# Kernel optimization log

Measured on AMD Instinct MI355X. Metric: run time of the kernel, lower is better.

## Reference

```python
import jax, jax.numpy as jnp
import numpy as np

D_MODEL, N_HEAD, D_HEAD, D_INNER = 1024, 16, 64, 4096
QLEN, MLEN, BATCH = 1024, 1024, 2
KLEN = QLEN + MLEN
LN_EPS = 1e-5


def layer_norm(x, g, b):
    m = jnp.mean(x, axis=-1, keepdims=True)
    v = jnp.mean((x - m) ** 2, axis=-1, keepdims=True)
    return g * (x - m) * jax.lax.rsqrt(v + LN_EPS) + b


def rel_shift(x):
    # x: [q, k, b, n] -> Transformer-XL relative shift
    q, k = x.shape[0], x.shape[1]
    zero_pad = jnp.zeros((q, 1) + x.shape[2:], dtype=x.dtype)
    x_padded = jnp.concatenate([zero_pad, x], axis=1)          # [q, k+1, b, n]
    x_padded = x_padded.reshape((k + 1, q) + x.shape[2:])      # [k+1, q, b, n]
    return x_padded[1:].reshape(x.shape)


def setup_inputs() -> dict:
    key = jax.random.key(0)
    ks = jax.random.split(key, 12)
    s = 0.02
    return {
        "w": jax.random.normal(ks[0], (QLEN, BATCH, D_MODEL), jnp.float32),
        "mems": jax.random.normal(ks[1], (MLEN, BATCH, D_MODEL), jnp.float32),
        "r_emb": jax.random.normal(ks[2], (KLEN, N_HEAD, D_HEAD), jnp.float32) * s,
        "r_w_bias": jax.random.normal(ks[3], (N_HEAD, D_HEAD), jnp.float32) * s,
        "r_bias": jax.random.normal(ks[4], (KLEN, N_HEAD), jnp.float32) * s,
        "qkv_w": jax.random.normal(ks[5], (3 * N_HEAD * D_HEAD, D_MODEL), jnp.float32) * s,
        "o_w": jax.random.normal(ks[6], (D_MODEL, N_HEAD * D_HEAD), jnp.float32) * s,
        "ln1_g": jnp.ones((D_MODEL,), jnp.float32),
        "ln1_b": jnp.zeros((D_MODEL,), jnp.float32),
        "ff_w1": jax.random.normal(ks[7], (D_INNER, D_MODEL), jnp.float32) * s,
        "ff_b1": jnp.zeros((D_INNER,), jnp.float32),
        "ff_w2": jax.random.normal(ks[8], (D_MODEL, D_INNER), jnp.float32) * s,
        "ff_b2": jnp.zeros((D_MODEL,), jnp.float32),
        "ln2_g": jnp.ones((D_MODEL,), jnp.float32),
        "ln2_b": jnp.zeros((D_MODEL,), jnp.float32),
    }


def reference(w, mems, r_emb, r_w_bias, r_bias, qkv_w, o_w, ln1_g, ln1_b,
              ff_w1, ff_b1, ff_w2, ff_b2, ln2_g, ln2_b):
    qlen, nbatch = w.shape[0], w.shape[1]
    scale = 1.0 / (D_HEAD ** 0.5)

    # --- RelLearnableMultiHeadAttn (post-lnorm, dropout=0 / eval) ---
    cat = jnp.concatenate([mems, w], axis=0)                       # [klen, b, d_model]
    w_heads = jnp.einsum('kbd,ed->kbe', cat, qkv_w)                # [klen, b, 3*n*h]
    w_head_q, w_head_k, w_head_v = jnp.split(w_heads, 3, axis=-1)
    klen = w_head_k.shape[0]
    w_head_q = w_head_q[-qlen:].reshape(qlen, nbatch, N_HEAD, D_HEAD)
    w_head_k = w_head_k.reshape(klen, nbatch, N_HEAD, D_HEAD)
    w_head_v = w_head_v.reshape(klen, nbatch, N_HEAD, D_HEAD)

    r_emb_k = r_emb[-klen:]                                        # [klen, n, h]
    r_bias_k = r_bias[-klen:]                                      # [klen, n]

    rw_head_q = w_head_q + r_w_bias[None, None]                    # [q, b, n, h]
    AC = jnp.einsum('ibnd,jbnd->ijbn', rw_head_q, w_head_k)        # [q, k, b, n]
    B_ = jnp.einsum('ibnd,jnd->ijbn', w_head_q, r_emb_k)           # [q, k, b, n]
    D_ = r_bias_k[None, :, None, :]                                # [1, k, 1, n]
    BD = rel_shift(B_ + D_)

    attn_score = (AC + BD) * scale
    # causal mask with memory: key j attendable iff j <= i + mlen
    mlen = klen - qlen
    i = jnp.arange(qlen)[:, None]
    j = jnp.arange(klen)[None, :]
    mask = j > (i + mlen)                                          # [q, k]
    attn_score = jnp.where(mask[:, :, None, None], -1e30, attn_score)

    attn_prob = jax.nn.softmax(attn_score, axis=1)
    attn_vec = jnp.einsum('ijbn,jbnd->ibnd', attn_prob, w_head_v)
    attn_vec = attn_vec.reshape(qlen, nbatch, N_HEAD * D_HEAD)
    attn_out = jnp.einsum('ibe,de->ibd', attn_vec, o_w)
    h = layer_norm(w + attn_out, ln1_g, ln1_b)

    # --- PositionwiseFF (post-lnorm) ---
    inner = jax.nn.relu(jnp.einsum('ibd,fd->ibf', h, ff_w1) + ff_b1)
    ff_out = jnp.einsum('ibf,df->ibd', inner, ff_w2) + ff_b2
    out = layer_norm(h + ff_out, ln2_g, ln2_b)
    return out
```

## Files before the change

### kernel.cpp

```cpp
#include <hip/hip_runtime.h>
#include <math.h>

#define DM    1024
#define NH    16
#define DH    64
#define DI    4096
#define QL    1024
#define MLN   1024
#define BATCH 2
#define KL    2048
#define RPAD  2304

typedef unsigned short u16;
typedef short s16x8 __attribute__((ext_vector_type(8)));
typedef float f32x4 __attribute__((ext_vector_type(4)));

__device__ __forceinline__ u16 f2bf(float f) {
    union { float f; unsigned u; } v; v.f = f;
    unsigned u = v.u;
    unsigned r = (u + 0x7FFFu + ((u >> 16) & 1u)) >> 16;
    return (u16)r;
}
__device__ __forceinline__ u16 f2bf_fast(float f) {
    union { float f; unsigned u; } v; v.f = f;
    return (u16)((v.u + 0x8000u) >> 16);
}
__device__ __forceinline__ float bf2f(u16 h) {
    union { unsigned u; float f; } v; v.u = ((unsigned)h) << 16;
    return v.f;
}

__device__ __forceinline__ void gl2lds16(const void* g, void* l) {
    __builtin_amdgcn_global_load_lds(
        (const __attribute__((address_space(1))) void*)g,
        (__attribute__((address_space(3))) void*)l, 16, 0, 0);
}

__global__ __launch_bounds__(256) void cvt_multi(
    const float* __restrict__ a0, const float* __restrict__ a1,
    const float* __restrict__ a2, const float* __restrict__ a3,
    u16* __restrict__ o0, u16* __restrict__ o1,
    u16* __restrict__ o2, u16* __restrict__ o3) {
    int i = blockIdx.x * 256 + threadIdx.x;
    int stride = gridDim.x * 256;
    for (; i < 3145728; i += stride) {
        const float* src; u16* dst; int k;
        if (i < 786432)       { src = a0; dst = o0; k = i; }
        else if (i < 1048576) { src = a1; dst = o1; k = i - 786432; }
        else if (i < 2097152) { src = a2; dst = o2; k = i - 1048576; }
        else                  { src = a3; dst = o3; k = i - 2097152; }
        float4 v = ((const float4*)src)[k];
        ushort4 o = {f2bf(v.x), f2bf(v.y), f2bf(v.z), f2bf(v.w)};
        ((ushort4*)dst)[k] = o;
    }
}

__global__ __launch_bounds__(256) void cvt_cat(const float* __restrict__ mems,
                                               const float* __restrict__ w,
                                               u16* __restrict__ cat) {
    int id = blockIdx.x * 256 + threadIdx.x;
    int c4 = (id & 255) * 4;
    int row = id >> 8;
    int b = row >> 11, kpos = row & 2047;
    const float* src = (kpos < QL)
        ? mems + ((size_t)kpos * BATCH + b) * DM + c4
        : w + ((size_t)(kpos - QL) * BATCH + b) * DM + c4;
    float4 v = *(const float4*)src;
    ushort4 o = {f2bf(v.x), f2bf(v.y), f2bf(v.z), f2bf(v.w)};
    *(ushort4*)(cat + (size_t)row * DM + c4) = o;
}

__global__ __launch_bounds__(256) void rcvt(const float* __restrict__ r_emb,
                                            u16* __restrict__ rh) {
    int id = blockIdx.x * 256 + threadIdx.x;
    int n = blockIdx.y;
    int jj = id >> 3, gs = id & 7;
    s16x8 o;
    if (jj < KL) {
        int gl = (gs - jj) & 7;
        const float* s = r_emb + (size_t)jj * DM + n * 64 + gl * 8;
#pragma unroll
        for (int k = 0; k < 8; ++k) o[k] = (short)f2bf(s[k]);
    } else {
#pragma unroll
        for (int k = 0; k < 8; ++k) o[k] = 0;
    }
    *(s16x8*)(rh + ((size_t)n * RPAD + jj) * 64 + gs * 8) = o;
}

__global__ __launch_bounds__(256) void rb2_prep(const float* __restrict__ r_emb,
                                                const float* __restrict__ r_w_bias,
                                                const float* __restrict__ r_bias,
                                                float* __restrict__ rb2) {
    int jj = blockIdx.x * 256 + threadIdx.x;
    int n = blockIdx.y;
    if (jj >= RPAD) return;
    float v = 0.0f;
    if (jj < KL) {
        float dot = 0.0f;
#pragma unroll 8
        for (int d = 0; d < 64; ++d)
            dot += r_w_bias[n * 64 + d] * r_emb[(size_t)jj * DM + n * 64 + d];
        v = 0.125f * (r_bias[jj * NH + n] - dot);
    }
    rb2[n * RPAD + jj] = v;
}

template <int BN, int FLAGS>
__global__ __launch_bounds__(256) void gemm_s(const u16* __restrict__ A,
                                              const u16* __restrict__ B,
                                              float* __restrict__ Cf,
                                              u16* __restrict__ Cb,
                                              u16* __restrict__ Qo,
                                              u16* __restrict__ Ko,
                                              u16* __restrict__ Vo,
                                              const float* __restrict__ bias,
                                              int M, int N_out, int K) {
    constexpr int WN = BN / 2;
    constexpr int TN = WN / 16;
    __shared__ u16 As[128 * 32];
    __shared__ u16 Bs[BN * 32];

    const int t = threadIdx.x;
    const int lane = t & 63, wid = t >> 6;
    const int wm = wid >> 1, wn = wid & 1;
    const int lr = lane & 15, quad = lane >> 4;
    const int m_blk = blockIdx.y * 128;
    const int n_blk = blockIdx.x * BN;
    const int srow = t >> 2;
    const int skc  = (t & 3) * 8;

    f32x4 acc[4][TN];
#pragma unroll
    for (int i = 0; i < 4; ++i)
#pragma unroll
        for (int j = 0; j < TN; ++j) acc[i][j] = (f32x4)0.0f;

    for (int k0 = 0; k0 < K; k0 += 32) {
        __syncthreads();
        gl2lds16(A + (size_t)(m_blk + srow) * K + k0 + skc, As + wid * 512);
        gl2lds16(A + (size_t)(m_blk + 64 + srow) * K + k0 + skc, As + 2048 + wid * 512);
        gl2lds16(B + (size_t)(n_blk + srow) * K + k0 + skc, Bs + wid * 512);
        if (BN == 128)
            gl2lds16(B + (size_t)(n_blk + 64 + srow) * K + k0 + skc, Bs + 2048 + wid * 512);
        __syncthreads();

        s16x8 a[4], b[TN];
#pragma unroll
        for (int i = 0; i < 4; ++i)
            a[i] = *(const s16x8*)(As + (wm * 64 + i * 16 + lr) * 32 + quad * 8);
#pragma unroll
        for (int j = 0; j < TN; ++j)
            b[j] = *(const s16x8*)(Bs + (wn * WN + j * 16 + lr) * 32 + quad * 8);
#pragma unroll
        for (int i = 0; i < 4; ++i)
#pragma unroll
            for (int j = 0; j < TN; ++j)
                acc[i][j] = __builtin_amdgcn_mfma_f32_16x16x32_bf16(
                    a[i], b[j], acc[i][j], 0, 0, 0);
    }

#pragma unroll
    for (int i = 0; i < 4; ++i) {
#pragma unroll
        for (int j = 0; j < TN; ++j) {
            int row0 = m_blk + wm * 64 + i * 16 + quad * 4;
            int col  = n_blk + wn * WN + j * 16 + lr;
            if (FLAGS & 8) {
                int b_ = row0 >> 11, kpos = row0 & 2047;
                if (col < 1024) {
                    if (kpos >= QL) {
                        u16* q = Qo + ((size_t)(b_ * QL + kpos - QL)) * 1024 + col;
#pragma unroll
                        for (int r = 0; r < 4; ++r) q[r * 1024] = f2bf(acc[i][j][r]);
                    }
                } else if (col < 2048) {
                    int d = col & 63, nh = (col >> 6) & 15;
                    size_t base = ((size_t)((b_ * 16 + nh) * 16 + (kpos >> 7))) * 8192;
#pragma unroll
                    for (int r = 0; r < 4; ++r) {
                        int jl = (kpos & 127) + r;
                        Ko[base + jl * 64 + (((d >> 3) + jl) & 7) * 8 + (d & 7)] =
                            f2bf(acc[i][j][r]);
                    }
                } else {
                    int d = col & 63, nh = (col >> 6) & 15;
                    int jl = kpos & 127;
                    size_t base = ((size_t)((b_ * 16 + nh) * 16 + (kpos >> 7))) * 8192
                                  + d * 128 + (((jl >> 3) + d) & 15) * 8 + (jl & 7);
                    ushort4 o = {f2bf(acc[i][j][0]), f2bf(acc[i][j][1]),
                                 f2bf(acc[i][j][2]), f2bf(acc[i][j][3])};
                    *(ushort4*)(Vo + base) = o;
                }
            } else {
                float bv = (FLAGS & 2) ? bias[col] : 0.0f;
#pragma unroll
                for (int r = 0; r < 4; ++r) {
                    float v = acc[i][j][r] + bv;
                    if (FLAGS & 4) v = fmaxf(v, 0.0f);
                    size_t idx = (size_t)(row0 + r) * N_out + col;
                    if (FLAGS & 1) Cb[idx] = f2bf(v);
                    else           Cf[idx] = v;
                }
            }
        }
    }
}

__global__ __launch_bounds__(256, 2) void flash_attn(
    const u16* __restrict__ Qb, const u16* __restrict__ Kh,
    const u16* __restrict__ Vt2, const u16* __restrict__ rh,
    const float* __restrict__ r_w_bias, const float* __restrict__ rb2,
    u16* __restrict__ av) {
    const int bn = blockIdx.x & 31;
    const int i0 = (blockIdx.x >> 5) * 64;
    const int b = bn >> 4, n = bn & 15;
    const int t = threadIdx.x;
    const int lane = t & 63, w = t >> 6;
    const int lr = lane & 15, quad = lane >> 4;

    __shared__ __align__(16) u16 Ks[128 * 64];
    __shared__ __align__(16) u16 Vs[64 * 128];
    __shared__ __align__(16) u16 Rs[192 * 64];
    __shared__ __align__(16) u16 Pw_all[4 * 16 * 136];
    u16* Pw = Pw_all + w * (16 * 136);

    const int wrow0 = i0 + w * 16;

    s16x8 qw[2];
#pragma unroll
    for (int ks = 0; ks < 2; ++ks) {
        const u16* qp = Qb + ((size_t)(b * QL + wrow0 + lr)) * 1024 + n * 64 + ks * 32 + quad * 8;
        s16x8 qv = *(const s16x8*)qp;
        s16x8 o;
#pragma unroll
        for (int k = 0; k < 8; ++k) {
            float f = bf2f((u16)qv[k]) + r_w_bias[n * 64 + ks * 32 + quad * 8 + k];
            o[k] = (short)f2bf(f * 0.125f);
        }
        qw[ks] = o;
    }

    f32x4 O[4];
    float m_r[4], l_r[4];
#pragma unroll
    for (int x = 0; x < 4; ++x) {
        O[x] = (f32x4)0.0f;
        m_r[x] = -INFINITY;
        l_r[x] = 0.0f;
    }

    const u16* Kt0 = Kh + (size_t)bn * 16 * 8192;
    const u16* Vt0 = Vt2 + (size_t)bn * 16 * 8192;
    const int jend = i0 + 64 + MLN;

    for (int j0 = 0; j0 < jend; j0 += 128) {
        const int jjbase_blk = j0 + 960 - i0;
        __syncthreads();
        {
            const u16* Ksrc = Kt0 + (size_t)(j0 >> 7) * 8192;
            const u16* Vsrc = Vt0 + (size_t)(j0 >> 7) * 8192;
            const u16* Rsrc = rh + ((size_t)n * RPAD + jjbase_blk) * 64;
#pragma unroll
            for (int k = 0; k < 4; ++k)
                gl2lds16(Ksrc + (w * 4 + k) * 512 + lane * 8, Ks + (w * 4 + k) * 512);
#pragma unroll
            for (int k = 0; k < 4; ++k)
                gl2lds16(Vsrc + (w * 4 + k) * 512 + lane * 8, Vs + (w * 4 + k) * 512);
#pragma unroll
            for (int k = 0; k < 6; ++k)
                gl2lds16(Rsrc + (w * 6 + k) * 512 + lane * 8, Rs + (w * 6 + k) * 512);
        }
        __syncthreads();

        f32x4 bacc[9];
#pragma unroll
        for (int c = 0; c < 9; ++c) bacc[c] = (f32x4)0.0f;
#pragma unroll
        for (int ks = 0; ks < 2; ++ks) {
#pragma unroll
            for (int c = 0; c < 9; ++c) {
                int row = c * 16 + lr + 48 - 16 * w;
                s16x8 rf = *(const s16x8*)(Rs + row * 64 + (((ks * 4 + quad) + row) & 7) * 8);
                bacc[c] = __builtin_amdgcn_mfma_f32_16x16x32_bf16(qw[ks], rf, bacc[c], 0, 0, 0);
            }
        }
#pragma unroll
        for (int c = 0; c < 9; ++c) {
            int jj = jjbase_blk + 48 - 16 * w + c * 16 + lr;
            float rv = rb2[n * RPAD + jj];
            bacc[c][0] += rv; bacc[c][1] += rv; bacc[c][2] += rv; bacc[c][3] += rv;
        }
        f32x4 sacc[8];
#pragma unroll
        for (int r = 0; r < 4; ++r) {
            int rho = quad * 4 + r;
            int lrt_src = (lr + rho + 1) & 15;
            int up = lrt_src > rho;
            int addr = (((lane & 48) | ((lr + 15 - rho) & 15)) << 2);
#pragma unroll
            for (int nt = 0; nt < 8; ++nt) {
                float v = up ? bacc[nt + 1][r] : bacc[nt][r];
                sacc[nt][r] = __int_as_float(
                    __builtin_amdgcn_ds_bpermute(addr, __float_as_int(v)));
            }
        }

#pragma unroll
        for (int ks = 0; ks < 2; ++ks) {
#pragma unroll
            for (int nt = 0; nt < 8; ++nt) {
                int jloc = nt * 16 + lr;
                s16x8 kf = *(const s16x8*)(Ks + jloc * 64 + (((ks * 4 + quad) + jloc) & 7) * 8);
                sacc[nt] = __builtin_amdgcn_mfma_f32_16x16x32_bf16(qw[ks], kf, sacc[nt], 0, 0, 0);
            }
        }
#pragma unroll
        for (int nt = 0; nt < 8; ++nt) {
            int j = j0 + nt * 16 + lr;
#pragma unroll
            for (int r = 0; r < 4; ++r) {
                int i = wrow0 + quad * 4 + r;
                if (j > i + MLN) sacc[nt][r] = -INFINITY;
            }
        }

        float mx[4];
#pragma unroll
        for (int r = 0; r < 4; ++r) {
            mx[r] = sacc[0][r];
#pragma unroll
            for (int nt = 1; nt < 8; ++nt) mx[r] = fmaxf(mx[r], sacc[nt][r]);
        }
#pragma unroll
        for (int msk = 1; msk <= 8; msk <<= 1)
#pragma unroll
            for (int r = 0; r < 4; ++r)
                mx[r] = fmaxf(mx[r], __shfl_xor(mx[r], msk, 64));
        float al[4], mn[4];
#pragma unroll
        for (int r = 0; r < 4; ++r) {
            mn[r] = fmaxf(m_r[r], mx[r]);
            al[r] = __expf(m_r[r] - mn[r]);
            m_r[r] = mn[r];
#pragma unroll
            for (int dt = 0; dt < 4; ++dt) O[dt][r] *= al[r];
        }
        float ps[4] = {0.0f, 0.0f, 0.0f, 0.0f};
#pragma unroll
        for (int nt = 0; nt < 8; ++nt)
#pragma unroll
            for (int r = 0; r < 4; ++r) {
                float p = __expf(sacc[nt][r] - mn[r]);
                ps[r] += p;
                Pw[(quad * 4 + r) * 136 + nt * 16 + lr] = f2bf_fast(p);
            }
#pragma unroll
        for (int msk = 1; msk <= 8; msk <<= 1)
#pragma unroll
            for (int r = 0; r < 4; ++r) ps[r] += __shfl_xor(ps[r], msk, 64);
#pragma unroll
        for (int r = 0; r < 4; ++r) l_r[r] = l_r[r] * al[r] + ps[r];

#pragma unroll
        for (int ks2 = 0; ks2 < 4; ++ks2) {
            s16x8 ap = *(const s16x8*)(Pw + lr * 136 + ks2 * 32 + quad * 8);
#pragma unroll
            for (int dt = 0; dt < 4; ++dt) {
                int d = dt * 16 + lr;
                s16x8 vb = *(const s16x8*)(Vs + d * 128 + (((ks2 * 4 + quad) + d) & 15) * 8);
                O[dt] = __builtin_amdgcn_mfma_f32_16x16x32_bf16(ap, vb, O[dt], 0, 0, 0);
            }
        }
    }

    float rL[4];
#pragma unroll
    for (int r = 0; r < 4; ++r) rL[r] = 1.0f / l_r[r];
#pragma unroll
    for (int dt = 0; dt < 4; ++dt)
#pragma unroll
        for (int r = 0; r < 4; ++r) {
            int i = wrow0 + quad * 4 + r;
            av[(size_t)(i * 2 + b) * DM + n * 64 + dt * 16 + lr] = f2bf(O[dt][r] * rL[r]);
        }
}

__global__ __launch_bounds__(256) void ln_fused(
    const float* __restrict__ x1, const float* __restrict__ x2,
    const float* __restrict__ gw, const float* __restrict__ bw,
    float* __restrict__ outf, u16* __restrict__ outb, int mode) {
    const int row = blockIdx.x, t = threadIdx.x, lane = t & 63, wv = t >> 6;
    __shared__ float red[8];
    float x[4];
    float s = 0.0f, s2 = 0.0f;
#pragma unroll
    for (int r = 0; r < 4; ++r) {
        int c = t + r * 256;
        float v = x1[(size_t)row * DM + c] + x2[(size_t)row * DM + c];
        x[r] = v;
        s += v;
        s2 += v * v;
    }
#pragma unroll
    for (int o = 32; o; o >>= 1) {
        s  += __shfl_xor(s, o, 64);
        s2 += __shfl_xor(s2, o, 64);
    }
    if (lane == 0) { red[wv] = s; red[4 + wv] = s2; }
    __syncthreads();
    s  = red[0] + red[1] + red[2] + red[3];
    s2 = red[4] + red[5] + red[6] + red[7];
    float mean = s * (1.0f / DM);
    float var  = s2 * (1.0f / DM) - mean * mean;
    float rstd = rsqrtf(var + 1e-5f);
#pragma unroll
    for (int r = 0; r < 4; ++r) {
        int c = t + r * 256;
        float y = gw[c] * (x[r] - mean) * rstd + bw[c];
        size_t idx = (size_t)row * DM + c;
        if (mode & 1) outf[idx] = y;
        if (mode & 2) outb[idx] = f2bf(y);
    }
}

extern "C" void kernel_launch(void* const* d_in, const int* in_sizes, int n_in,
                              void* d_out, int out_size, void* d_ws, size_t ws_size,
                              hipStream_t stream) {
    const float* w        = (const float*)d_in[0];
    const float* mems     = (const float*)d_in[1];
    const float* r_emb    = (const float*)d_in[2];
    const float* r_w_bias = (const float*)d_in[3];
    const float* r_bias   = (const float*)d_in[4];
    const float* qkv_w    = (const float*)d_in[5];
    const float* o_w      = (const float*)d_in[6];
    const float* ln1_g    = (const float*)d_in[7];
    const float* ln1_b    = (const float*)d_in[8];
    const float* ff_w1    = (const float*)d_in[9];
    const float* ff_b1    = (const float*)d_in[10];
    const float* ff_w2    = (const float*)d_in[11];
    const float* ff_b2    = (const float*)d_in[12];
    const float* ln2_g    = (const float*)d_in[13];
    const float* ln2_b    = (const float*)d_in[14];
    float* out = (float*)d_out;

    char* ws = (char*)d_ws;
    size_t off = 0;
    auto alloc = [&](size_t bytes) {
        size_t o = off;
        off += (bytes + 255) & ~(size_t)255;
        return o;
    };
    u16* cat_bf   = (u16*)(ws + alloc((size_t)KL * BATCH * DM * 2));
    u16* qkvw_bf  = (u16*)(ws + alloc((size_t)3 * NH * DH * DM * 2));
    u16* ow_bf    = (u16*)(ws + alloc((size_t)DM * NH * DH * 2));
    u16* w1_bf    = (u16*)(ws + alloc((size_t)DI * DM * 2));
    u16* w2_bf    = (u16*)(ws + alloc((size_t)DM * DI * 2));
    u16* rh_bf    = (u16*)(ws + alloc((size_t)NH * RPAD * 64 * 2));
    float* rb2    = (float*)(ws + alloc((size_t)NH * RPAD * 4));
    u16* Qb_bf    = (u16*)(ws + alloc((size_t)BATCH * QL * 1024 * 2));
    u16* Kh_bf    = (u16*)(ws + alloc((size_t)32 * 16 * 8192 * 2));
    u16* Vt2_bf   = (u16*)(ws + alloc((size_t)32 * 16 * 8192 * 2));
    u16* av_bf    = (u16*)(ws + alloc((size_t)QL * BATCH * DM * 2));
    float* ao_f   = (float*)(ws + alloc((size_t)QL * BATCH * DM * 4));
    float* h_f    = (float*)(ws + alloc((size_t)QL * BATCH * DM * 4));
    u16* h_bf     = (u16*)(ws + alloc((size_t)QL * BATCH * DM * 2));
    u16* inner_bf = (u16*)(ws + alloc((size_t)QL * BATCH * DI * 2));
    float* ffo_f  = (float*)(ws + alloc((size_t)QL * BATCH * DM * 4));
    (void)ws_size; (void)in_sizes; (void)n_in; (void)out_size;

    cvt_cat<<<4096, 256, 0, stream>>>(mems, w, cat_bf);
    cvt_multi<<<2048, 256, 0, stream>>>(qkv_w, o_w, ff_w1, ff_w2,
                                        qkvw_bf, ow_bf, w1_bf, w2_bf);
    rcvt<<<dim3(72, 16), 256, 0, stream>>>(r_emb, rh_bf);
    rb2_prep<<<dim3(9, 16), 256, 0, stream>>>(r_emb, r_w_bias, r_bias, rb2);

    gemm_s<128, 8><<<dim3(3072 / 128, (KL * BATCH) / 128), 256, 0, stream>>>(
        cat_bf, qkvw_bf, nullptr, nullptr, Qb_bf, Kh_bf, Vt2_bf, nullptr,
        KL * BATCH, 3072, DM);

    flash_attn<<<512, 256, 0, stream>>>(Qb_bf, Kh_bf, Vt2_bf, rh_bf,
                                        r_w_bias, rb2, av_bf);

    gemm_s<64, 0><<<dim3(DM / 64, (QL * BATCH) / 128), 256, 0, stream>>>(
        av_bf, ow_bf, ao_f, nullptr, nullptr, nullptr, nullptr, nullptr,
        QL * BATCH, DM, DM);

    ln_fused<<<QL * BATCH, 256, 0, stream>>>(w, ao_f, ln1_g, ln1_b, h_f, h_bf, 3);

    gemm_s<128, 1 | 2 | 4><<<dim3(DI / 128, (QL * BATCH) / 128), 256, 0, stream>>>(
        h_bf, w1_bf, nullptr, inner_bf, nullptr, nullptr, nullptr, ff_b1,
        QL * BATCH, DI, DM);

    gemm_s<64, 2><<<dim3(DM / 64, (QL * BATCH) / 128), 256, 0, stream>>>(
        inner_bf, w2_bf, ffo_f, nullptr, nullptr, nullptr, nullptr, ff_b2,
        QL * BATCH, DM, DI);

    ln_fused<<<QL * BATCH, 256, 0, stream>>>(h_f, ffo_f, ln2_g, ln2_b, out, nullptr, 1);
}
```

Before: 376.4 us.

## Split-K the output and FF2 projections and reduce partials inside layernorm

Adds a split-K GEMM kernel that writes two fp32 partial products into the no-longer-needed Kh buffer. The o_w projection and the second feed-forward GEMM now use it with a 2-way K split. The layernorm kernels sum the partials and add the bias. This doubles the block count for these 2048x1024 GEMMs (256 to 512 blocks) to fill more CUs, and moves the bias into the layernorm. The cost is extra fp32 partial traffic, and the simpler GEMM kernel uses single-buffered 32-wide K steps, which may be less efficient per block.

```diff
diff --git a/kernel.cpp b/kernel.cpp
--- a/kernel.cpp
+++ b/kernel.cpp
@@ -207,6 +207,67 @@
     }
 }
 
+template <int SPLIT>
+__global__ __launch_bounds__(256) void gemm_sk(const u16* __restrict__ A,
+                                               const u16* __restrict__ B,
+                                               float* __restrict__ P,
+                                               int M, int N_out, int K) {
+    __shared__ u16 As[128 * 32];
+    __shared__ u16 Bs[64 * 32];
+
+    const int t = threadIdx.x;
+    const int lane = t & 63, wid = t >> 6;
+    const int wm = wid >> 1, wn = wid & 1;
+    const int lr = lane & 15, quad = lane >> 4;
+    const int m_blk = blockIdx.y * 128;
+    const int n_blk = blockIdx.x * 64;
+    const int kz = blockIdx.z;
+    const int Kc = K / SPLIT;
+    const int kbeg = kz * Kc, kend = kbeg + Kc;
+    const int srow = t >> 2;
+    const int skc  = (t & 3) * 8;
+
+    f32x4 acc[4][2];
+#pragma unroll
+    for (int i = 0; i < 4; ++i)
+#pragma unroll
+        for (int j = 0; j < 2; ++j) acc[i][j] = (f32x4)0.0f;
+
+    for (int k0 = kbeg; k0 < kend; k0 += 32) {
+        __syncthreads();
+        gl2lds16(A + (size_t)(m_blk + srow) * K + k0 + skc, As + wid * 512);
+        gl2lds16(A + (size_t)(m_blk + 64 + srow) * K + k0 + skc, As + 2048 + wid * 512);
+        gl2lds16(B + (size_t)(n_blk + srow) * K + k0 + skc, Bs + wid * 512);
+        __syncthreads();
+
+        s16x8 a[4], b[2];
+#pragma unroll
+        for (int i = 0; i < 4; ++i)
+            a[i] = *(const s16x8*)(As + (wm * 64 + i * 16 + lr) * 32 + quad * 8);
+#pragma unroll
+        for (int j = 0; j < 2; ++j)
+            b[j] = *(const s16x8*)(Bs + (wn * 32 + j * 16 + lr) * 32 + quad * 8);
+#pragma unroll
+        for (int i = 0; i < 4; ++i)
+#pragma unroll
+            for (int j = 0; j < 2; ++j)
+                acc[i][j] = __builtin_amdgcn_mfma_f32_16x16x32_bf16(
+                    a[i], b[j], acc[i][j], 0, 0, 0);
+    }
+
+    float* Pz = P + (size_t)kz * M * N_out;
+#pragma unroll
+    for (int i = 0; i < 4; ++i)
+#pragma unroll
+        for (int j = 0; j < 2; ++j) {
+            int row0 = m_blk + wm * 64 + i * 16 + quad * 4;
+            int col  = n_blk + wn * 32 + j * 16 + lr;
+#pragma unroll
+            for (int r = 0; r < 4; ++r)
+                Pz[(size_t)(row0 + r) * N_out + col] = acc[i][j][r];
+        }
+}
+
 __global__ __launch_bounds__(256, 2) void flash_attn(
     const u16* __restrict__ Qb, const u16* __restrict__ Kh,
     const u16* __restrict__ Vt2, const u16* __restrict__ rh,
@@ -386,18 +447,22 @@
         }
 }
 
-__global__ __launch_bounds__(256) void ln_fused(
-    const float* __restrict__ x1, const float* __restrict__ x2,
+__global__ __launch_bounds__(256) void ln_fused_k(
+    const float* __restrict__ x1, const float* __restrict__ P,
+    const float* __restrict__ bias,
     const float* __restrict__ gw, const float* __restrict__ bw,
     float* __restrict__ outf, u16* __restrict__ outb, int mode) {
     const int row = blockIdx.x, t = threadIdx.x, lane = t & 63, wv = t >> 6;
+    const size_t MN = (size_t)QL * BATCH * DM;
     __shared__ float red[8];
     float x[4];
     float s = 0.0f, s2 = 0.0f;
 #pragma unroll
     for (int r = 0; r < 4; ++r) {
         int c = t + r * 256;
-        float v = x1[(size_t)row * DM + c] + x2[(size_t)row * DM + c];
+        size_t idx = (size_t)row * DM + c;
+        float v = x1[idx] + P[idx] + P[MN + idx];
+        if (bias) v += bias[c];
         x[r] = v;
         s += v;
         s2 += v * v;
@@ -462,12 +527,12 @@
     u16* Kh_bf    = (u16*)(ws + alloc((size_t)32 * 16 * 8192 * 2));
     u16* Vt2_bf   = (u16*)(ws + alloc((size_t)32 * 16 * 8192 * 2));
     u16* av_bf    = (u16*)(ws + alloc((size_t)QL * BATCH * DM * 2));
-    float* ao_f   = (float*)(ws + alloc((size_t)QL * BATCH * DM * 4));
     float* h_f    = (float*)(ws + alloc((size_t)QL * BATCH * DM * 4));
     u16* h_bf     = (u16*)(ws + alloc((size_t)QL * BATCH * DM * 2));
     u16* inner_bf = (u16*)(ws + alloc((size_t)QL * BATCH * DI * 2));
-    float* ffo_f  = (float*)(ws + alloc((size_t)QL * BATCH * DM * 4));
     (void)ws_size; (void)in_sizes; (void)n_in; (void)out_size;
+
+    float* Pk = (float*)Kh_bf;
 
     cvt_cat<<<4096, 256, 0, stream>>>(mems, w, cat_bf);
     cvt_multi<<<2048, 256, 0, stream>>>(qkv_w, o_w, ff_w1, ff_w2,
@@ -482,19 +547,19 @@
     flash_attn<<<512, 256, 0, stream>>>(Qb_bf, Kh_bf, Vt2_bf, rh_bf,
                                         r_w_bias, rb2, av_bf);
 
-    gemm_s<64, 0><<<dim3(DM / 64, (QL * BATCH) / 128), 256, 0, stream>>>(
-        av_bf, ow_bf, ao_f, nullptr, nullptr, nullptr, nullptr, nullptr,
-        QL * BATCH, DM, DM);
-
-    ln_fused<<<QL * BATCH, 256, 0, stream>>>(w, ao_f, ln1_g, ln1_b, h_f, h_bf, 3);
+    gemm_sk<2><<<dim3(DM / 64, (QL * BATCH) / 128, 2), 256, 0, stream>>>(
+        av_bf, ow_bf, Pk, QL * BATCH, DM, DM);
+
+    ln_fused_k<<<QL * BATCH, 256, 0, stream>>>(w, Pk, nullptr, ln1_g, ln1_b,
+                                               h_f, h_bf, 3);
 
     gemm_s<128, 1 | 2 | 4><<<dim3(DI / 128, (QL * BATCH) / 128), 256, 0, stream>>>(
         h_bf, w1_bf, nullptr, inner_bf, nullptr, nullptr, nullptr, ff_b1,
         QL * BATCH, DI, DM);
 
-    gemm_s<64, 2><<<dim3(DM / 64, (QL * BATCH) / 128), 256, 0, stream>>>(
-        inner_bf, w2_bf, ffo_f, nullptr, nullptr, nullptr, nullptr, ff_b2,
-        QL * BATCH, DM, DI);
-
-    ln_fused<<<QL * BATCH, 256, 0, stream>>>(h_f, ffo_f, ln2_g, ln2_b, out, nullptr, 1);
-}
+    gemm_sk<2><<<dim3(DM / 64, (QL * BATCH) / 128, 2), 256, 0, stream>>>(
+        inner_bf, w2_bf, Pk, QL * BATCH, DM, DI);
+
+    ln_fused_k<<<QL * BATCH, 256, 0, stream>>>(h_f, Pk, ff_b2, ln2_g, ln2_b,
+                                               out, nullptr, 1);
+}
```

New measurement: 344.9 us. 8.4% less time.
